# Optimization experiments

Hardware: AMD Instinct MI355X
Metric: run time of the kernel (lower is better)

The kernel has to match this reference:

```python
import math
import jax, jax.numpy as jnp
import numpy as np

N_HEAD = 16
N_EMBD = 2048
HEAD_DIM = N_EMBD // N_HEAD  # 128
ROPE_BASE = 10000.0
EPS = 1e-12  # F.normalize eps


def setup_inputs() -> dict:
    key = jax.random.key(0)
    ks = jax.random.split(key, 5)
    B, T, C = 2, 2048, N_EMBD
    s = 0.02
    return {
        "x": jax.random.normal(ks[0], (B, T, C), jnp.float32),
        "Wq": jax.random.normal(ks[1], (C, C), jnp.float32) * s,
        "Wk": jax.random.normal(ks[2], (C, C), jnp.float32) * s,
        "Wv": jax.random.normal(ks[3], (C, C), jnp.float32) * s,
        "Wo": jax.random.normal(ks[4], (C, C), jnp.float32) * s,
        "qk_scale": jnp.ones((HEAD_DIM,), jnp.float32) / math.sqrt(N_EMBD),
    }


def _rope(x, cos, sin):
    # x: [B,T,H,D], cos/sin: [T, D/2] broadcast as [1,T,1,D/2]
    d = x.shape[-1] // 2
    x1, x2 = x[..., :d], x[..., d:]
    c = cos[None, :, None, :]
    s = sin[None, :, None, :]
    return jnp.concatenate([x1 * c + x2 * s, -x1 * s + x2 * c], axis=-1)


def reference(x, Wq, Wk, Wv, Wo, qk_scale):
    B, T, C = x.shape
    H, D = N_HEAD, HEAD_DIM

    q = (x @ Wq.T).reshape(B, T, H, D)
    k = (x @ Wk.T).reshape(B, T, H, D)
    v = (x @ Wv.T).reshape(B, T, H, D)

    # L2-normalize over head_dim, then per-channel scale (scaler() = param * sqrt(n_embd))
    scale_vec = qk_scale * math.sqrt(N_EMBD)  # == 1.0 at init
    q = scale_vec * (q / jnp.maximum(jnp.linalg.norm(q, axis=-1, keepdims=True), EPS))
    k = scale_vec * (k / jnp.maximum(jnp.linalg.norm(k, axis=-1, keepdims=True), EPS))

    # rotary embeddings (half-split, non-interleaved)
    inv_freq = 1.0 / (ROPE_BASE ** (jnp.arange(0, D, 2, dtype=jnp.float32) / D))
    freqs = jnp.arange(T, dtype=jnp.float32)[:, None] * inv_freq[None, :]  # [T, D/2]
    cos, sin = jnp.cos(freqs), jnp.sin(freqs)
    q = _rope(q, cos, sin)
    k = _rope(k, cos, sin)

    # causal SDPA with scale = sqrt(head_dim) (as in the source)
    scores = jnp.einsum("bthd,bshd->bhts", q, k) * math.sqrt(D)  # [B,H,T,T]
    causal = jnp.tril(jnp.ones((T, T), bool))
    scores = jnp.where(causal[None, None], scores, -jnp.inf)
    attn = jax.nn.softmax(scores, axis=-1)
    y = jnp.einsum("bhts,bshd->bthd", attn, v).reshape(B, T, C)
    return y @ Wo.T
```

## Files before the change

kernel.cpp:

```cpp
#include <hip/hip_runtime.h>
#include <math.h>

typedef _Float16 f16;
typedef _Float16 f16x2 __attribute__((ext_vector_type(2)));
typedef _Float16 f16x4 __attribute__((ext_vector_type(4)));
typedef _Float16 f16x8 __attribute__((ext_vector_type(8)));
typedef __fp16 fp16x2 __attribute__((ext_vector_type(2)));
typedef float f32x4 __attribute__((ext_vector_type(4)));
typedef float f32x16 __attribute__((ext_vector_type(16)));
typedef unsigned int u32;

#define T_ 2048
#define H_ 16
#define C_ 2048

__device__ __forceinline__ void gload_lds16(const f16* g, f16* l) {
  __builtin_amdgcn_global_load_lds((const __attribute__((address_space(1))) u32*)g,
                                   (__attribute__((address_space(3))) u32*)l, 16, 0, 0);
}

__device__ __forceinline__ u32 pkk(float x, float y) {
  union { fp16x2 h; u32 u; } z;
  z.h = __builtin_amdgcn_cvt_pkrtz(x, y);
  return z.u;
}

__global__ __launch_bounds__(256) void cast_all_kernel(
    const float* __restrict__ x, const float* __restrict__ wq, const float* __restrict__ wk,
    const float* __restrict__ wv, const float* __restrict__ wo,
    f16* __restrict__ xh, f16* __restrict__ wqh, f16* __restrict__ wkh,
    f16* __restrict__ wvh, f16* __restrict__ woh) {
  int b = blockIdx.x;
  const float* src; f16* dst; size_t off;
  if (b < 8192) { src = x; dst = xh; off = (size_t)b * 1024; }
  else {
    int s = (b - 8192) >> 12, bb = (b - 8192) & 4095;
    off = (size_t)bb * 1024;
    if (s == 0) { src = wq; dst = wqh; }
    else if (s == 1) { src = wk; dst = wkh; }
    else if (s == 2) { src = wv; dst = wvh; }
    else { src = wo; dst = woh; }
  }
  size_t i = off + (size_t)threadIdx.x * 4;
  float4 v = *(const float4*)&src[i];
  f16x4 o; o[0] = (f16)v.x; o[1] = (f16)v.y; o[2] = (f16)v.z; o[3] = (f16)v.w;
  *(f16x4*)&dst[i] = o;
}

template<typename OutT>
__device__ __forceinline__ void gemm128(const f16* __restrict__ A, const f16* __restrict__ Bm,
                                        OutT* __restrict__ Cm, f16* As, f16* Bs,
                                        int brow, int bcol) {
  const int K = 2048, N = 2048;
  const int tid = threadIdx.x, l = tid & 63, w = tid >> 6;
  const int lr = l & 15, lg = l >> 4;
  const int wr = (w >> 1) * 64, wc = (w & 1) * 64;
  const int srow = l >> 2, scol = (l & 3) * 8;
  const f16* gA0 = A + (size_t)(brow + w * 32 + srow) * K + scol;
  const f16* gA1 = gA0 + (size_t)16 * K;
  const f16* gB0 = Bm + (size_t)(bcol + w * 32 + srow) * K + scol;
  const f16* gB1 = gB0 + (size_t)16 * K;
  f16* lA0 = &As[(w * 32 + 0) * 32];
  f16* lA1 = &As[(w * 32 + 16) * 32];
  f16* lB0 = &Bs[(w * 32 + 0) * 32];
  f16* lB1 = &Bs[(w * 32 + 16) * 32];
  f32x4 acc[4][4] = {};
  for (int kt = 0; kt < K; kt += 32) {
    gload_lds16(gA0 + kt, lA0);
    gload_lds16(gA1 + kt, lA1);
    gload_lds16(gB0 + kt, lB0);
    gload_lds16(gB1 + kt, lB1);
    __syncthreads();
    f16x8 af[4], bf[4];
#pragma unroll
    for (int m = 0; m < 4; ++m) af[m] = *(const f16x8*)&As[(wr + m * 16 + lr) * 32 + lg * 8];
#pragma unroll
    for (int n = 0; n < 4; ++n) bf[n] = *(const f16x8*)&Bs[(wc + n * 16 + lr) * 32 + lg * 8];
#pragma unroll
    for (int m = 0; m < 4; ++m)
#pragma unroll
      for (int n = 0; n < 4; ++n)
        acc[m][n] = __builtin_amdgcn_mfma_f32_16x16x32_f16(af[m], bf[n], acc[m][n], 0, 0, 0);
    __syncthreads();
  }
#pragma unroll
  for (int m = 0; m < 4; ++m) {
    int row0 = brow + wr + m * 16 + lg * 4;
#pragma unroll
    for (int n = 0; n < 4; ++n) {
      int col = bcol + wc + n * 16 + lr;
#pragma unroll
      for (int j = 0; j < 4; ++j)
        Cm[(size_t)(row0 + j) * N + col] = (OutT)acc[m][n][j];
    }
  }
}

__global__ __launch_bounds__(256) void gemm_qkv_kernel(
    const f16* __restrict__ A, const f16* __restrict__ Wq, const f16* __restrict__ Wk,
    const f16* __restrict__ Wv, f16* __restrict__ Qo, f16* __restrict__ Ko, f16* __restrict__ Vo) {
  __shared__ f16 As[4096], Bs[4096];
  const f16* Bm; f16* Cm;
  if (blockIdx.z == 0) { Bm = Wq; Cm = Qo; }
  else if (blockIdx.z == 1) { Bm = Wk; Cm = Ko; }
  else { Bm = Wv; Cm = Vo; }
  int lin = blockIdx.y * 32 + blockIdx.x;
  int swz = (lin & 7) * 64 + (lin >> 3);
  gemm128<f16>(A, Bm, Cm, As, Bs, (swz & 31) * 128, (swz >> 5) * 128);
}

__global__ __launch_bounds__(256) void gemm_out_kernel(
    const f16* __restrict__ A, const f16* __restrict__ Wo, float* __restrict__ Cm) {
  __shared__ f16 As[4096], Bs[4096];
  int lin = blockIdx.y * 32 + blockIdx.x;
  int swz = (lin & 7) * 64 + (lin >> 3);
  gemm128<float>(A, Wo, Cm, As, Bs, (swz & 31) * 128, (swz >> 5) * 128);
}

__global__ __launch_bounds__(256) void normrope_kernel(f16* __restrict__ qp, f16* __restrict__ kp,
                                                       const float* __restrict__ qk_scale) {
  int w = threadIdx.x >> 6, l = threadIdx.x & 63;
  f16* q = blockIdx.y == 0 ? qp : kp;
  float fac = blockIdx.y == 0 ? 512.0f : 45.254833995939045f;
  int row = blockIdx.x * 4 + w;
  int t = (row >> 4) & (T_ - 1);
  size_t base = (size_t)row * 128;
  float x1 = (float)q[base + l], x2 = (float)q[base + 64 + l];
  float ss = x1 * x1 + x2 * x2;
#pragma unroll
  for (int m = 1; m < 64; m <<= 1) ss += __shfl_xor(ss, m);
  float inv = 1.0f / fmaxf(sqrtf(ss), 1e-12f);
  float sc1 = qk_scale[l] * fac;
  float sc2 = qk_scale[l + 64] * fac;
  float s1 = x1 * inv * sc1, s2 = x2 * inv * sc2;
  float invf = exp2f(-(float)l * 0.20762050593046013f);
  float ang = (float)t * invf;
  float sn, cs; sincosf(ang, &sn, &cs);
  q[base + l] = (f16)(s1 * cs + s2 * sn);
  q[base + 64 + l] = (f16)(-s1 * sn + s2 * cs);
}

#define VSTR 68
__global__ __launch_bounds__(256, 2) void attn_kernel(
    const f16* __restrict__ Q, const f16* __restrict__ K, const f16* __restrict__ V,
    f16* __restrict__ Y, f16* __restrict__ Op, float* __restrict__ ml) {
  __shared__ f16 Ks[2][64 * 128];
  __shared__ f16 Vt[2][128 * VSTR];
  const int tid = threadIdx.x, l = tid & 63, w = tid >> 6;
  const int lq = l & 31, hi = l >> 5;
  const int bh = blockIdx.x / 40;
  const int cidx = blockIdx.x - bh * 40;
  int qi, j;
  if (cidx < 4)       { qi = cidx;                  j = 0; }
  else if (cidx < 12) { qi = 4 + ((cidx - 4) >> 1); j = (cidx - 4) & 1; }
  else if (cidx < 24) { qi = 8 + (cidx - 12) / 3;   j = (cidx - 12) % 3; }
  else                { qi = 12 + ((cidx - 24) >> 2); j = (cidx - 24) & 3; }
  const int nch = (qi >> 2) + 1;
  const bool multi = nch > 1;
  const int qb = qi * 128;
  const int s0kv = j * 512;
  const int endkv = min(s0kv + 512, qb + 128);
  const int nt = (endkv - s0kv) >> 6;
  const int tbase = s0kv >> 6;
  const int lastit = qi * 2 + (w >> 1);
  int cid = 0;
  if (multi) {
    int pre = (qi < 8) ? (qi - 4) * 2 : (qi < 12 ? 8 + (qi - 8) * 3 : 20 + (qi - 12) * 4);
    cid = bh * 36 + pre + j;
  }
  const int b = bh >> 4, h = bh & 15;
  const size_t hb = ((size_t)b * T_ * H_ + h) * 128;
  const int qw = qb + w * 32;
  const int q = qw + lq;

  f16x8 qB[8];
  {
    const f16* qp = Q + hb + (size_t)q * 2048 + hi * 8;
#pragma unroll
    for (int dc = 0; dc < 8; ++dc) qB[dc] = *(const f16x8*)(qp + dc * 16);
  }

  const int vp2 = tid & 31, vdg = (tid >> 5) * 8;
  f16x8 vr0a, vr1a, vr0b, vr1b;

  auto stageK = [&](int kv0, int buf) {
#pragma unroll
    for (int i = 0; i < 4; ++i) {
      int row_l = i * 4 + (l >> 4);
      const f16* kg = K + hb + (size_t)(kv0 + w * 16 + row_l) * 2048 + (((l & 15) ^ row_l) << 3);
      gload_lds16(kg, &Ks[buf][(w * 16 + i * 4) * 128]);
    }
  };
  auto loadV = [&](int kv0) {
    const f16* vsrc = V + hb + (size_t)(kv0 + 2 * vp2) * 2048;
    vr0a = *(const f16x8*)(vsrc + vdg);
    vr1a = *(const f16x8*)(vsrc + 2048 + vdg);
    vr0b = *(const f16x8*)(vsrc + vdg + 64);
    vr1b = *(const f16x8*)(vsrc + 2048 + vdg + 64);
  };
  auto writeV = [&](int buf) {
#pragma unroll
    for (int jj = 0; jj < 8; ++jj) {
      union { f16x2 h2; u32 u; } p0, p1;
      p0.h2[0] = vr0a[jj]; p0.h2[1] = vr1a[jj];
      *(u32*)&Vt[buf][(vdg + jj) * VSTR + 2 * vp2] = p0.u;
      p1.h2[0] = vr0b[jj]; p1.h2[1] = vr1b[jj];
      *(u32*)&Vt[buf][(vdg + 64 + jj) * VSTR + 2 * vp2] = p1.u;
    }
  };

  stageK(s0kv, 0);
  loadV(s0kv);
  asm volatile("s_waitcnt vmcnt(0)" ::: "memory");
  writeV(0);
  __syncthreads();

  float mreg = -INFINITY, rsum = 0.f;
  f32x16 o0 = {}, o1 = {}, o2 = {}, o3 = {};

  for (int it = 0; it < nt; ++it) {
    const int cur = it & 1;
    const int kv0 = s0kv + it * 64;
    const bool havenext = (it + 1 < nt);
    if (havenext) { stageK(kv0 + 64, cur ^ 1); loadV(kv0 + 64); }

    const int ti = tbase + it;
    if (ti <= lastit) {
      const char* kB = (const char*)&Ks[cur][0];
      const int rowoff = lq * 256, kmask = (lq & 15) * 16;
      f32x16 s0 = {}, s1 = {};
      __builtin_amdgcn_s_setprio(1);
#pragma unroll
      for (int dc = 0; dc < 8; ++dc) {
        f16x8 kf = *(const f16x8*)(kB + rowoff + ((dc * 32 + hi * 16) ^ kmask));
        s0 = __builtin_amdgcn_mfma_f32_32x32x16_f16(kf, qB[dc], s0, 0, 0, 0);
      }
#pragma unroll
      for (int dc = 0; dc < 8; ++dc) {
        f16x8 kf = *(const f16x8*)(kB + 8192 + rowoff + ((dc * 32 + hi * 16) ^ kmask));
        s1 = __builtin_amdgcn_mfma_f32_32x32x16_f16(kf, qB[dc], s1, 0, 0, 0);
      }
      __builtin_amdgcn_s_setprio(0);
      if (ti == lastit) {
#pragma unroll
        for (int r = 0; r < 16; ++r) {
          int crow = (r & 3) + 8 * (r >> 2) + 4 * hi;
          s0[r] = (kv0 + crow <= q) ? s0[r] : -INFINITY;
          s1[r] = (kv0 + 32 + crow <= q) ? s1[r] : -INFINITY;
        }
      }
      float t8[8];
#pragma unroll
      for (int r = 0; r < 8; ++r) t8[r] = fmaxf(fmaxf(s0[r], s0[r + 8]), fmaxf(s1[r], s1[r + 8]));
#pragma unroll
      for (int off = 4; off > 0; off >>= 1)
#pragma unroll
        for (int r = 0; r < off; ++r) t8[r] = fmaxf(t8[r], t8[r + off]);
      float pm = fmaxf(t8[0], __shfl_xor(t8[0], 32));
      if (multi) {
        float mn = fmaxf(mreg, pm);
        float al = __expf(mreg - mn);
        o0 *= al; o1 *= al; o2 *= al; o3 *= al;
        rsum *= al; mreg = mn;
      } else if (__any(pm > mreg + 8.0f)) {
        float mn = fmaxf(mreg, pm);
        float al = __expf(mreg - mn);
        o0 *= al; o1 *= al; o2 *= al; o3 *= al;
        rsum *= al; mreg = mn;
      }
      float sum = 0.f;
#pragma unroll
      for (int r = 0; r < 16; ++r) { float e = __expf(s0[r] - mreg); s0[r] = e; sum += e; }
#pragma unroll
      for (int r = 0; r < 16; ++r) { float e = __expf(s1[r] - mreg); s1[r] = e; sum += e; }
      sum += __shfl_xor(sum, 32);
      rsum += sum;
      __builtin_amdgcn_s_setprio(1);
#define PVSTEP(SV, BB, KS)                                                          \
      {                                                                             \
        u32 a0 = pkk(SV[8*BB+0], SV[8*BB+1]);                                       \
        u32 a1 = pkk(SV[8*BB+2], SV[8*BB+3]);                                       \
        u32 b0 = pkk(SV[8*BB+4], SV[8*BB+5]);                                       \
        u32 b1 = pkk(SV[8*BB+6], SV[8*BB+7]);                                       \
        u32 r0 = __shfl_xor(hi ? a0 : b0, 32);                                      \
        u32 r1 = __shfl_xor(hi ? a1 : b1, 32);                                      \
        union { u32 u[4]; f16x8 v; } pf;                                            \
        pf.u[0] = hi ? r0 : a0; pf.u[1] = hi ? r1 : a1;                             \
        pf.u[2] = hi ? b0 : r0; pf.u[3] = hi ? b1 : r1;                             \
        const f16* vb = &Vt[cur][lq * VSTR + (KS) * 16 + hi * 8];                   \
        o0 = __builtin_amdgcn_mfma_f32_32x32x16_f16(*(const f16x8*)(vb), pf.v, o0, 0, 0, 0); \
        o1 = __builtin_amdgcn_mfma_f32_32x32x16_f16(*(const f16x8*)(vb + 32 * VSTR), pf.v, o1, 0, 0, 0); \
        o2 = __builtin_amdgcn_mfma_f32_32x32x16_f16(*(const f16x8*)(vb + 64 * VSTR), pf.v, o2, 0, 0, 0); \
        o3 = __builtin_amdgcn_mfma_f32_32x32x16_f16(*(const f16x8*)(vb + 96 * VSTR), pf.v, o3, 0, 0, 0); \
      }
      PVSTEP(s0, 0, 0)
      PVSTEP(s0, 1, 1)
      PVSTEP(s1, 0, 2)
      PVSTEP(s1, 1, 3)
#undef PVSTEP
      __builtin_amdgcn_s_setprio(0);
    }
    if (havenext) {
      asm volatile("s_waitcnt vmcnt(0)" ::: "memory");
      writeV(cur ^ 1);
      __syncthreads();
    }
  }

  if (!multi) {
    float inv = 1.0f / rsum;
    const size_t yb = ((size_t)(b * T_ + q)) * 2048 + h * 128;
#define OSTORE(OV, DT)                                                   \
    {                                                                    \
      _Pragma("unroll")                                                  \
      for (int g = 0; g < 4; ++g) {                                      \
        f16x4 pk;                                                        \
        pk[0] = (f16)(OV[g * 4 + 0] * inv); pk[1] = (f16)(OV[g * 4 + 1] * inv); \
        pk[2] = (f16)(OV[g * 4 + 2] * inv); pk[3] = (f16)(OV[g * 4 + 3] * inv); \
        *(f16x4*)&Y[yb + (DT) * 32 + g * 8 + 4 * hi] = pk;               \
      }                                                                  \
    }
    OSTORE(o0, 0) OSTORE(o1, 1) OSTORE(o2, 2) OSTORE(o3, 3)
#undef OSTORE
  } else {
    const size_t ob = (size_t)cid * 16384 + (size_t)(w * 32 + lq) * 128;
#define OSTORE(OV, DT)                                                   \
    {                                                                    \
      _Pragma("unroll")                                                  \
      for (int g = 0; g < 4; ++g) {                                      \
        f16x4 pk;                                                        \
        pk[0] = (f16)OV[g * 4 + 0]; pk[1] = (f16)OV[g * 4 + 1];          \
        pk[2] = (f16)OV[g * 4 + 2]; pk[3] = (f16)OV[g * 4 + 3];          \
        *(f16x4*)&Op[ob + (DT) * 32 + g * 8 + 4 * hi] = pk;              \
      }                                                                  \
    }
    OSTORE(o0, 0) OSTORE(o1, 1) OSTORE(o2, 2) OSTORE(o3, 3)
#undef OSTORE
    if (hi == 0) {
      ml[(size_t)cid * 256 + (w * 32 + lq) * 2] = mreg;
      ml[(size_t)cid * 256 + (w * 32 + lq) * 2 + 1] = rsum;
    }
  }
}

__global__ __launch_bounds__(256) void merge_kernel(const f16* __restrict__ Op,
                                                    const float* __restrict__ ml,
                                                    f16* __restrict__ Y) {
  const int g = blockIdx.x;
  const int bh = g / 12, qi = 4 + (g - 12 * (g / 12));
  const int b = bh >> 4, h = bh & 15;
  const int nch = (qi >> 2) + 1;
  const int pre = (qi < 8) ? (qi - 4) * 2 : (qi < 12 ? 8 + (qi - 8) * 3 : 20 + (qi - 12) * 4);
  const int cid0 = bh * 36 + pre;
  const int row = threadIdx.x >> 1;
  const int dh = (threadIdx.x & 1) * 64;
  float mc[4], lc[4], wgt[4];
  float M = -INFINITY;
#pragma unroll
  for (int c = 0; c < 4; ++c)
    if (c < nch) {
      mc[c] = ml[(size_t)(cid0 + c) * 256 + row * 2];
      lc[c] = ml[(size_t)(cid0 + c) * 256 + row * 2 + 1];
      M = fmaxf(M, mc[c]);
    }
  float lsum = 0.f;
#pragma unroll
  for (int c = 0; c < 4; ++c)
    if (c < nch) { wgt[c] = __expf(mc[c] - M); lsum += lc[c] * wgt[c]; }
  float inv = 1.0f / lsum;
#pragma unroll
  for (int c = 0; c < 4; ++c)
    if (c < nch) wgt[c] *= inv;
  const int t = qi * 128 + row;
  const size_t yb = ((size_t)(b * T_ + t)) * 2048 + h * 128 + dh;
  const size_t rb = (size_t)row * 128 + dh;
#pragma unroll
  for (int dblk = 0; dblk < 64; dblk += 8) {
    float acc[8] = {};
#pragma unroll
    for (int c = 0; c < 4; ++c)
      if (c < nch) {
        f16x8 v = *(const f16x8*)&Op[(size_t)(cid0 + c) * 16384 + rb + dblk];
#pragma unroll
        for (int k = 0; k < 8; ++k) acc[k] += wgt[c] * (float)v[k];
      }
    f16x8 o;
#pragma unroll
    for (int k = 0; k < 8; ++k) o[k] = (f16)acc[k];
    *(f16x8*)&Y[yb + dblk] = o;
  }
}

extern "C" void kernel_launch(void* const* d_in, const int* in_sizes, int n_in,
                              void* d_out, int out_size, void* d_ws, size_t ws_size,
                              hipStream_t stream) {
  const float* x  = (const float*)d_in[0];
  const float* Wq = (const float*)d_in[1];
  const float* Wk = (const float*)d_in[2];
  const float* Wv = (const float*)d_in[3];
  const float* Wo = (const float*)d_in[4];
  const float* qk_scale = (const float*)d_in[5];
  float* out = (float*)d_out;
  char* ws = (char*)d_ws;

  f16* xh  = (f16*)(ws);
  f16* wqh = (f16*)(ws + 16777216);
  f16* wkh = (f16*)(ws + 25165824);
  f16* wvh = (f16*)(ws + 33554432);
  f16* woh = (f16*)(ws + 41943040);
  f16* qh  = (f16*)(ws + 50331648);
  f16* kh  = (f16*)(ws + 67108864);
  f16* vh  = (f16*)(ws + 83886080);
  f16* yh  = (f16*)(ws + 100663296);
  f16*   Op  = (f16*)(ws);
  float* mlp = (float*)(ws + 37748736);

  cast_all_kernel<<<dim3(24576), dim3(256), 0, stream>>>(x, Wq, Wk, Wv, Wo, xh, wqh, wkh, wvh, woh);
  gemm_qkv_kernel<<<dim3(32, 16, 3), dim3(256), 0, stream>>>(xh, wqh, wkh, wvh, qh, kh, vh);
  normrope_kernel<<<dim3(16384, 2), dim3(256), 0, stream>>>(qh, kh, qk_scale);
  attn_kernel<<<dim3(1280), dim3(256), 0, stream>>>(qh, kh, vh, yh, Op, mlp);
  merge_kernel<<<dim3(384), dim3(256), 0, stream>>>(Op, mlp, yh);
  gemm_out_kernel<<<dim3(32, 16), dim3(256), 0, stream>>>(yh, woh, out);
}
```

Measured before the change: 380.8 us.

## Halve attention KV tile to 32 rows and swizzle block-to-work mapping

The attention kernel now processes 32 KV rows per iteration instead of 64, which halves the shared-memory K and V buffers and the per-iteration MFMA, softmax and PV work. The causal last-tile index is now computed per wave at the finer granularity. The block index is also permuted so that neighbouring blocks spread across different (batch, head) chunks, aiming at better load balance or cache locality. The cost is twice as many iterations, each with its own barrier and global-load latency, so there is less work to hide that latency.

```diff
diff --git a/kernel.cpp b/kernel.cpp
--- a/kernel.cpp
+++ b/kernel.cpp
@@ -140,16 +140,18 @@
   q[base + 64 + l] = (f16)(-s1 * sn + s2 * cs);
 }
 
-#define VSTR 68
+#define VSTR 36
 __global__ __launch_bounds__(256, 2) void attn_kernel(
     const f16* __restrict__ Q, const f16* __restrict__ K, const f16* __restrict__ V,
     f16* __restrict__ Y, f16* __restrict__ Op, float* __restrict__ ml) {
-  __shared__ f16 Ks[2][64 * 128];
+  __shared__ f16 Ks[2][32 * 128];
   __shared__ f16 Vt[2][128 * VSTR];
   const int tid = threadIdx.x, l = tid & 63, w = tid >> 6;
   const int lq = l & 31, hi = l >> 5;
-  const int bh = blockIdx.x / 40;
-  const int cidx = blockIdx.x - bh * 40;
+  const int bid = blockIdx.x;
+  const int swzb = (bid & 7) * 160 + (bid >> 3);
+  const int bh = swzb / 40;
+  const int cidx = swzb - bh * 40;
   int qi, j;
   if (cidx < 4)       { qi = cidx;                  j = 0; }
   else if (cidx < 12) { qi = 4 + ((cidx - 4) >> 1); j = (cidx - 4) & 1; }
@@ -160,9 +162,9 @@
   const int qb = qi * 128;
   const int s0kv = j * 512;
   const int endkv = min(s0kv + 512, qb + 128);
-  const int nt = (endkv - s0kv) >> 6;
-  const int tbase = s0kv >> 6;
-  const int lastit = qi * 2 + (w >> 1);
+  const int nt = (endkv - s0kv) >> 5;
+  const int tbase = s0kv >> 5;
+  const int lastit = qi * 4 + w;
   int cid = 0;
   if (multi) {
     int pre = (qi < 8) ? (qi - 4) * 2 : (qi < 12 ? 8 + (qi - 8) * 3 : 20 + (qi - 12) * 4);
@@ -180,32 +182,30 @@
     for (int dc = 0; dc < 8; ++dc) qB[dc] = *(const f16x8*)(qp + dc * 16);
   }
 
-  const int vp2 = tid & 31, vdg = (tid >> 5) * 8;
-  f16x8 vr0a, vr1a, vr0b, vr1b;
+  const int vpr = tid & 15;
+  const int vdg = (tid >> 4) * 8;
+  f16x8 vr0a, vr1a;
 
   auto stageK = [&](int kv0, int buf) {
 #pragma unroll
-    for (int i = 0; i < 4; ++i) {
-      int row_l = i * 4 + (l >> 4);
-      const f16* kg = K + hb + (size_t)(kv0 + w * 16 + row_l) * 2048 + (((l & 15) ^ row_l) << 3);
-      gload_lds16(kg, &Ks[buf][(w * 16 + i * 4) * 128]);
+    for (int i = 0; i < 2; ++i) {
+      int rbase = w * 8 + i * 4;
+      int row_in = rbase + (l >> 4);
+      const f16* kg = K + hb + (size_t)(kv0 + row_in) * 2048 + (((l & 15) ^ (row_in & 15)) << 3);
+      gload_lds16(kg, &Ks[buf][rbase * 128]);
     }
   };
   auto loadV = [&](int kv0) {
-    const f16* vsrc = V + hb + (size_t)(kv0 + 2 * vp2) * 2048;
-    vr0a = *(const f16x8*)(vsrc + vdg);
-    vr1a = *(const f16x8*)(vsrc + 2048 + vdg);
-    vr0b = *(const f16x8*)(vsrc + vdg + 64);
-    vr1b = *(const f16x8*)(vsrc + 2048 + vdg + 64);
+    const f16* vsrc = V + hb + (size_t)(kv0 + 2 * vpr) * 2048 + vdg;
+    vr0a = *(const f16x8*)(vsrc);
+    vr1a = *(const f16x8*)(vsrc + 2048);
   };
   auto writeV = [&](int buf) {
 #pragma unroll
     for (int jj = 0; jj < 8; ++jj) {
-      union { f16x2 h2; u32 u; } p0, p1;
+      union { f16x2 h2; u32 u; } p0;
       p0.h2[0] = vr0a[jj]; p0.h2[1] = vr1a[jj];
-      *(u32*)&Vt[buf][(vdg + jj) * VSTR + 2 * vp2] = p0.u;
-      p1.h2[0] = vr0b[jj]; p1.h2[1] = vr1b[jj];
-      *(u32*)&Vt[buf][(vdg + 64 + jj) * VSTR + 2 * vp2] = p1.u;
+      *(u32*)&Vt[buf][(vdg + jj) * VSTR + 2 * vpr] = p0.u;
     }
   };
 
@@ -220,38 +220,32 @@
 
   for (int it = 0; it < nt; ++it) {
     const int cur = it & 1;
-    const int kv0 = s0kv + it * 64;
+    const int kv0 = s0kv + it * 32;
     const bool havenext = (it + 1 < nt);
-    if (havenext) { stageK(kv0 + 64, cur ^ 1); loadV(kv0 + 64); }
+    if (havenext) { stageK(kv0 + 32, cur ^ 1); loadV(kv0 + 32); }
 
     const int ti = tbase + it;
     if (ti <= lastit) {
       const char* kB = (const char*)&Ks[cur][0];
       const int rowoff = lq * 256, kmask = (lq & 15) * 16;
-      f32x16 s0 = {}, s1 = {};
+      f32x16 s0 = {};
       __builtin_amdgcn_s_setprio(1);
 #pragma unroll
       for (int dc = 0; dc < 8; ++dc) {
         f16x8 kf = *(const f16x8*)(kB + rowoff + ((dc * 32 + hi * 16) ^ kmask));
         s0 = __builtin_amdgcn_mfma_f32_32x32x16_f16(kf, qB[dc], s0, 0, 0, 0);
       }
-#pragma unroll
-      for (int dc = 0; dc < 8; ++dc) {
-        f16x8 kf = *(const f16x8*)(kB + 8192 + rowoff + ((dc * 32 + hi * 16) ^ kmask));
-        s1 = __builtin_amdgcn_mfma_f32_32x32x16_f16(kf, qB[dc], s1, 0, 0, 0);
-      }
       __builtin_amdgcn_s_setprio(0);
       if (ti == lastit) {
 #pragma unroll
         for (int r = 0; r < 16; ++r) {
           int crow = (r & 3) + 8 * (r >> 2) + 4 * hi;
           s0[r] = (kv0 + crow <= q) ? s0[r] : -INFINITY;
-          s1[r] = (kv0 + 32 + crow <= q) ? s1[r] : -INFINITY;
         }
       }
       float t8[8];
 #pragma unroll
-      for (int r = 0; r < 8; ++r) t8[r] = fmaxf(fmaxf(s0[r], s0[r + 8]), fmaxf(s1[r], s1[r + 8]));
+      for (int r = 0; r < 8; ++r) t8[r] = fmaxf(s0[r], s0[r + 8]);
 #pragma unroll
       for (int off = 4; off > 0; off >>= 1)
 #pragma unroll
@@ -271,8 +265,6 @@
       float sum = 0.f;
 #pragma unroll
       for (int r = 0; r < 16; ++r) { float e = __expf(s0[r] - mreg); s0[r] = e; sum += e; }
-#pragma unroll
-      for (int r = 0; r < 16; ++r) { float e = __expf(s1[r] - mreg); s1[r] = e; sum += e; }
       sum += __shfl_xor(sum, 32);
       rsum += sum;
       __builtin_amdgcn_s_setprio(1);
@@ -295,8 +287,6 @@
       }
       PVSTEP(s0, 0, 0)
       PVSTEP(s0, 1, 1)
-      PVSTEP(s1, 0, 2)
-      PVSTEP(s1, 1, 3)
 #undef PVSTEP
       __builtin_amdgcn_s_setprio(0);
     }
```

Result: no change. 381.6 us (+0.2%).
